# Kernel tuning notes

Measured on AMD Instinct MI355X. Metric: run time of the kernel, lower is better.

## Reference

```python
import jax, jax.numpy as jnp
import numpy as np
import math

B, N, H, OUT = 32, 2048, 256, 128
K = 6            # knn_graph k
ALPHA = 0.2      # GCN2Conv alpha (beta=1 since theta/layer are None)
NEG = 0.2        # leaky_relu negative slope in ASAP
EPS = 1e-5       # batchnorm eps
RATIOS = (0.15, 0.25, 0.5)


def _scatter_add(vals, idx, n):
    # vals [B,E] or [B,E,h], idx [B,E] -> [B,n,...]
    b, e = idx.shape
    gi = (idx + jnp.arange(b)[:, None] * n).reshape(-1)
    flat = vals.reshape((b * e,) + vals.shape[2:])
    return jax.ops.segment_sum(flat, gi, num_segments=b * n).reshape((b, n) + vals.shape[2:])


def _scatter_max(vals, idx, n):
    b, e = idx.shape
    gi = (idx + jnp.arange(b)[:, None] * n).reshape(-1)
    flat = vals.reshape((b * e,) + vals.shape[2:])
    return jax.ops.segment_max(flat, gi, num_segments=b * n).reshape((b, n) + vals.shape[2:])


def _gather(x, idx):
    # x [B,n,...] or [B,n], idx [B,E]
    if x.ndim == 3:
        return jnp.take_along_axis(x, idx[..., None], axis=1)
    return jnp.take_along_axis(x, idx, axis=1)


def _knn_undirected(pos):
    # knn_graph(pos, k=6, loop=True) then to_undirected (coalesced via `valid` mask)
    b, n, _ = pos.shape
    d2 = jnp.sum((pos[:, :, None, :] - pos[:, None, :, :]) ** 2, axis=-1)  # [B,n,n]
    _, nbr = jax.lax.top_k(-d2, K)                # self included (dist 0)
    ctr = jnp.broadcast_to(jnp.arange(n)[None, :, None], (b, n, K)).reshape(b, n * K)
    nbr = nbr.reshape(b, n * K)
    src = jnp.concatenate([nbr, ctr], axis=1)     # symmetrize
    dst = jnp.concatenate([ctr, nbr], axis=1)
    key = src * n + dst
    order = jnp.argsort(key, axis=1)
    src = jnp.take_along_axis(src, order, axis=1)
    dst = jnp.take_along_axis(dst, order, axis=1)
    key = jnp.take_along_axis(key, order, axis=1)
    valid = jnp.concatenate([jnp.ones((b, 1), bool), key[:, 1:] != key[:, :-1]], axis=1)
    return src, dst, valid


def _edge_mlp(pos, src, dst, valid, W1, b1, g, be, m, v, W2, b2):
    # relu(MLP([1,32,1])(||p_i - p_j||)); BN in eval mode; self loops replaced by 1
    d = jnp.linalg.norm(_gather(pos, src) - _gather(pos, dst), axis=-1)  # [B,E]
    t = d[..., None] @ W1 + b1                       # [B,E,32]
    t = (t - m) * jax.lax.rsqrt(v + EPS) * g + be
    t = jax.nn.relu(t)
    w = jax.nn.relu((t @ W2 + b2)[..., 0])
    w = jnp.where(src == dst, 1.0, w)                # add_remaining_self_loops fill=1
    return jnp.where(valid, w, 0.0)                  # coalesce duplicate edges


def _gcn2(x, x0, src, dst, w, Wc):
    # GCN2Conv with beta=1, shared weights: ((1-a)*A_hat x + a*x0) @ W
    n = x.shape[1]
    deg = _scatter_add(w, dst, n)
    dis = jax.lax.rsqrt(jnp.maximum(deg, 1e-12))     # deg >= 1 (self loops)
    norm = _gather(dis, src) * w * _gather(dis, dst)
    agg = _scatter_add(norm[..., None] * _gather(x, src), dst, n)
    return ((1.0 - ALPHA) * agg + ALPHA * x0) @ Wc


def _asap(x, src, dst, valid, w, kpool, Wrel, brel, Wroot, Wlin, blin, Watt, batt,
          lW1, lb1, lW2, lW3, lb3):
    n = x.shape[1]
    # gnn_intra_cluster: GraphConv (add aggregation)
    x_pool = _scatter_add(w[..., None] * _gather(x, src), dst, n) @ Wrel + brel + x @ Wroot
    mj = _gather(x_pool, src)                                    # [B,E,H]
    x_q = _scatter_max(jnp.where(valid[..., None], mj, -jnp.inf), dst, n) @ Wlin + blin
    score = (jnp.concatenate([_gather(x_q, dst), mj], axis=-1) @ Watt + batt)[..., 0]
    score = jnp.where(valid, jax.nn.leaky_relu(score, NEG), -jnp.inf)
    smax = _scatter_max(score, dst, n)
    e = jnp.where(valid, jnp.exp(score - _gather(smax, dst)), 0.0)
    att = e / _gather(_scatter_add(e, dst, n), dst)
    xn = _scatter_add(att[..., None] * _gather(x, src), dst, n)
    # LEConv fitness (no edge weights; duplicates masked)
    a = (xn @ lW1 + lb1)[..., 0]
    bb = (xn @ lW2)[..., 0]
    msg = jnp.where(valid, _gather(a, src) - _gather(bb, dst), 0.0)
    fit = jax.nn.sigmoid(_scatter_add(msg, dst, n) + (xn @ lW3 + lb3)[..., 0])
    vals, idx = jax.lax.top_k(fit, kpool)
    return _gather(xn, idx) * vals[..., None], idx


def _forward(x, pos, conv_W, eW1, eb1, ebn_g, ebn_b, ebn_m, ebn_v, eW2, eb2,
             aWrel, abrel, aWroot, aWlin, ablin, aWatt, abatt,
             leW1, leb1, leW2, leW3, leb3, gW, gb, nW, nb):
    h = None
    readouts = []
    for s in range(4):
        src, dst, valid = _knn_undirected(pos)
        w = _edge_mlp(pos, src, dst, valid, eW1[s], eb1[s], ebn_g[s], ebn_b[s],
                      ebn_m[s], ebn_v[s], eW2[s], eb2[s])
        if s in (1, 2):
            readouts.append(jnp.concatenate([jnp.mean(h, axis=1), jnp.max(h, axis=1)], axis=-1))
        hin = x if s == 0 else h
        h = jax.nn.relu(_gcn2(hin, x, src, dst, w, conv_W[s]))
        if s < 3:
            kpool = math.ceil(RATIOS[s] * h.shape[1])
            h, idx = _asap(h, src, dst, valid, w, kpool, aWrel[s], abrel[s], aWroot[s],
                           aWlin[s], ablin[s], aWatt[s], abatt[s],
                           leW1[s], leb1[s], leW2[s], leW3[s], leb3[s])
            x = _gather(x, idx)
            pos = _gather(pos, idx)
    gate = jax.nn.softmax(h @ gW + gb, axis=1)      # attentional aggregation
    gp = jnp.sum(gate * (h @ nW + nb), axis=1)      # [B,OUT]
    return jnp.concatenate([gp, readouts[1], readouts[0]], axis=-1)


def setup_inputs() -> dict:
    key = jax.random.key(0)
    ks = iter(jax.random.split(key, 40))
    def rn(shape, scale=1.0):
        return scale * jax.random.normal(next(ks), shape, dtype=jnp.float32)
    return {
        "x": rn((B, N, H)),
        "pos": rn((B, N, 3)),
        "conv_W": rn((4, H, H), H ** -0.5),
        "eW1": rn((4, 1, 32)),
        "eb1": rn((4, 32), 0.1),
        "ebn_g": 1.0 + rn((4, 32), 0.1),
        "ebn_b": rn((4, 32), 0.1),
        "ebn_m": rn((4, 32), 0.1),
        "ebn_v": jnp.ones((4, 32), jnp.float32),
        "eW2": rn((4, 32, 1), 32 ** -0.5),
        "eb2": rn((4, 1), 0.1),
        "aWrel": rn((3, H, H), H ** -0.5),
        "abrel": rn((3, H), 0.1),
        "aWroot": rn((3, H, H), H ** -0.5),
        "aWlin": rn((3, H, H), H ** -0.5),
        "ablin": rn((3, H), 0.1),
        "aWatt": rn((3, 2 * H, 1), (2 * H) ** -0.5),
        "abatt": rn((3, 1), 0.1),
        "leW1": rn((3, H, 1), H ** -0.5),
        "leb1": rn((3, 1), 0.1),
        "leW2": rn((3, H, 1), H ** -0.5),
        "leW3": rn((3, H, 1), H ** -0.5),
        "leb3": rn((3, 1), 0.1),
        "gW": rn((H, 1), H ** -0.5),
        "gb": rn((1,), 0.1),
        "nW": rn((H, OUT), H ** -0.5),
        "nb": rn((OUT,), 0.1),
    }


def reference(x, pos, conv_W, eW1, eb1, ebn_g, ebn_b, ebn_m, ebn_v, eW2, eb2,
              aWrel, abrel, aWroot, aWlin, ablin, aWatt, abatt,
              leW1, leb1, leW2, leW3, leb3, gW, gb, nW, nb):
    return _forward(x, pos, conv_W, eW1, eb1, ebn_g, ebn_b, ebn_m, ebn_v, eW2, eb2,
                    aWrel, abrel, aWroot, aWlin, ablin, aWatt, abatt,
                    leW1, leb1, leW2, leW3, leb3, gW, gb, nW, nb)
```

## Files before the change

kernel.cpp:

```cpp
#include <hip/hip_runtime.h>
#include <hip/hip_bf16.h>
#include <math.h>

#define BB 32
#define NMAX 2048
#define HD 256
#define KNN 6
#define OUTD 128
#define NCH 4

typedef __hip_bfloat16 bf16;

__global__ void k_detect(const void* __restrict__ x, int* __restrict__ flag){
  __shared__ int cnt_s;
  if (threadIdx.x==0) cnt_s=0;
  __syncthreads();
  const unsigned short* u=(const unsigned short*)x;
  int c=0;
  for (int i=threadIdx.x;i<4096;i+=256){
    int e=(u[i]>>7)&0xFF;
    if (e>=0xC0) c++;
  }
  atomicAdd(&cnt_s,c);
  __syncthreads();
  if (threadIdx.x==0) flag[0]=(cnt_s>32)?1:0;
}

__device__ __forceinline__ float loadx(const void* x, int fl, size_t idx){
  if (fl) return ((const float*)x)[idx];
  unsigned short u=((const unsigned short*)x)[idx];
  return __uint_as_float(((unsigned)u)<<16);
}

__global__ void k_cvtx(const void* __restrict__ x, const int* __restrict__ flag,
                       float* __restrict__ Hf){
  int t=blockIdx.x*256+threadIdx.x;
  Hf[t]=loadx(x,flag[0],t);
}
__global__ void k_cvtpos(const void* __restrict__ pos, const int* __restrict__ flag,
                         float* __restrict__ posF){
  int t=blockIdx.x*256+threadIdx.x;
  if (t>=BB*NMAX*3) return;
  posF[t]=loadx(pos,flag[0],t);
}
struct WTab { const void* src[25]; int cnt[25]; int dst[25]; };
__global__ void k_cvtw(WTab tab, const int* __restrict__ flag, float* __restrict__ wsW){
  int seg=blockIdx.y;
  int t=blockIdx.x*256+threadIdx.x;
  if (t>=tab.cnt[seg]) return;
  wsW[tab.dst[seg]+t]=loadx(tab.src[seg],flag[0],t);
}

__global__ void k_initcum(int* __restrict__ cum){
  int t=blockIdx.x*256+threadIdx.x;
  if (t<BB*NMAX) cum[t]=t%NMAX;
}
__global__ void k_zero2(int* __restrict__ a, int* __restrict__ b, int n){
  int t=blockIdx.x*256+threadIdx.x;
  if (t<n){ a[t]=0; b[t]=0; }
}
__global__ void k_gatherpos(const float* __restrict__ posF, const int* __restrict__ cum,
                            float* __restrict__ posf, int n){
  int t=blockIdx.x*256+threadIdx.x;
  if (t>=BB*n*3) return;
  int c=t%3, i=(t/3)%n, b=t/(3*n);
  posf[t]=posF[((size_t)b*NMAX+cum[b*NMAX+i])*3+c];
}

__global__ void k_knn_part(const float* __restrict__ posf, double* __restrict__ dcand,
                           int* __restrict__ icand, int n){
  int b=blockIdx.z, ch=blockIdx.y;
  int i=blockIdx.x*256+threadIdx.x;
  const float* pp=posf+(size_t)b*n*3;
  int cs=(n+NCH-1)/NCH;
  int jlo=ch*cs, jhi=jlo+cs; if (jhi>n) jhi=n;
  double px=0.0,py=0.0,pz=0.0;
  if (i<n){ px=(double)pp[i*3]; py=(double)pp[i*3+1]; pz=(double)pp[i*3+2]; }
  double bd0=INFINITY,bd1=INFINITY,bd2=INFINITY,bd3=INFINITY,bd4=INFINITY,bd5=INFINITY;
  int   bi0=0x7fffffff,bi1=0x7fffffff,bi2=0x7fffffff,bi3=0x7fffffff,bi4=0x7fffffff,bi5=0x7fffffff;
  __shared__ double sx[256],sy[256],sz[256];
  for (int base=jlo;base<jhi;base+=256){
    int j=base+threadIdx.x;
    if (j<jhi){ sx[threadIdx.x]=(double)pp[j*3]; sy[threadIdx.x]=(double)pp[j*3+1]; sz[threadIdx.x]=(double)pp[j*3+2]; }
    __syncthreads();
    int lim=jhi-base; if (lim>256) lim=256;
    if (i<n){
      for (int t=0;t<lim;t++){
        double dx=__dsub_rn(px,sx[t]);
        double dy=__dsub_rn(py,sy[t]);
        double dz=__dsub_rn(pz,sz[t]);
        double d2=__dadd_rn(__dadd_rn(__dmul_rn(dx,dx),__dmul_rn(dy,dy)),__dmul_rn(dz,dz));
        if (d2<bd5){
          int id=base+t;
          if (d2<bd4){ bd5=bd4; bi5=bi4;
            if (d2<bd3){ bd4=bd3; bi4=bi3;
              if (d2<bd2){ bd3=bd2; bi3=bi2;
                if (d2<bd1){ bd2=bd1; bi2=bi1;
                  if (d2<bd0){ bd1=bd0; bi1=bi0; bd0=d2; bi0=id; }
                  else { bd1=d2; bi1=id; }
                } else { bd2=d2; bi2=id; }
              } else { bd3=d2; bi3=id; }
            } else { bd4=d2; bi4=id; }
          } else { bd5=d2; bi5=id; }
        }
      }
    }
    __syncthreads();
  }
  if (i<n){
    size_t o=(((size_t)b*NCH+ch)*n+i)*KNN;
    dcand[o+0]=bd0; dcand[o+1]=bd1; dcand[o+2]=bd2; dcand[o+3]=bd3; dcand[o+4]=bd4; dcand[o+5]=bd5;
    icand[o+0]=bi0; icand[o+1]=bi1; icand[o+2]=bi2; icand[o+3]=bi3; icand[o+4]=bi4; icand[o+5]=bi5;
  }
}

__global__ void k_knn_merge(const double* __restrict__ dcand, const int* __restrict__ icand,
                            int* __restrict__ nbr, int n){
  int t=blockIdx.x*256+threadIdx.x;
  if (t>=BB*n) return;
  int b=t/n, i=t-b*n;
  double cd[NCH*KNN]; int ci[NCH*KNN];
  #pragma unroll
  for (int ch=0;ch<NCH;ch++){
    size_t o=(((size_t)b*NCH+ch)*n+i)*KNN;
    #pragma unroll
    for (int k=0;k<KNN;k++){ cd[ch*KNN+k]=dcand[o+k]; ci[ch*KNN+k]=icand[o+k]; }
  }
  int* out=nbr+(size_t)t*KNN;
  #pragma unroll
  for (int k=0;k<KNN;k++){
    int best=0;
    #pragma unroll
    for (int q=1;q<NCH*KNN;q++){
      bool lt=(cd[q]<cd[best])||(cd[q]==cd[best]&&ci[q]<ci[best]);
      if (lt) best=q;
    }
    out[k]=ci[best];
    cd[best]=INFINITY; ci[best]=0x7fffffff;
  }
}

__global__ void k_edge(const float* __restrict__ posf, const int* __restrict__ nbr,
                       float* __restrict__ w1, float* __restrict__ w2,
                       unsigned char* __restrict__ val2,
                       const float* __restrict__ W1, const float* __restrict__ b1,
                       const float* __restrict__ g,  const float* __restrict__ be,
                       const float* __restrict__ m,  const float* __restrict__ v,
                       const float* __restrict__ W2, const float* __restrict__ b2p,
                       int n){
  int t=blockIdx.x*256+threadIdx.x;
  if (t>=BB*n*KNN) return;
  int k=t%KNN; int c=(t/KNN)%n; int b=t/(KNN*n);
  const int* nb=nbr+(size_t)b*n*KNN;
  int j=nb[c*KNN+k];
  bool dup=false;
  #pragma unroll
  for (int kk=0;kk<KNN;kk++) dup=dup||(nb[j*KNN+kk]==c);
  const float* pp=posf+(size_t)b*n*3;
  double dx=__dsub_rn((double)pp[c*3+0],(double)pp[j*3+0]);
  double dy=__dsub_rn((double)pp[c*3+1],(double)pp[j*3+1]);
  double dz=__dsub_rn((double)pp[c*3+2],(double)pp[j*3+2]);
  double d2=__dadd_rn(__dadd_rn(__dmul_rn(dx,dx),__dmul_rn(dy,dy)),__dmul_rn(dz,dz));
  float dd=(float)sqrt(d2);
  float wv;
  if (j==c) wv=1.0f;
  else {
    float acc=b2p[0];
    for (int q=0;q<32;q++){
      float tt=dd*W1[q]+b1[q];
      float r=1.0f/sqrtf(v[q]+1e-5f);
      tt=(tt-m[q])*r*g[q]+be[q];
      tt=fmaxf(tt,0.f);
      acc=fmaf(tt,W2[q],acc);
    }
    wv=fmaxf(acc,0.f);
  }
  w1[t]=wv;
  w2[t]=dup?0.f:wv;
  val2[t]=dup?0:1;
}

__global__ void k_csr_count(const int* __restrict__ nbr, int* __restrict__ cnt, int n){
  int t=blockIdx.x*256+threadIdx.x;
  if (t>=BB*n*KNN) return;
  int b=t/(n*KNN);
  atomicAdd(&cnt[b*n+nbr[t]],1);
}
__global__ void k_csr_scan(const int* __restrict__ cnt, int* __restrict__ offs, int n){
  int b=blockIdx.x, t=threadIdx.x;
  int L=(n+255)/256;
  __shared__ int ssum[256];
  int lo=t*L, hi=lo+L; if (hi>n) hi=n; if (lo>n) lo=n;
  int s=0;
  for (int i=lo;i<hi;i++) s+=cnt[b*n+i];
  ssum[t]=s;
  __syncthreads();
  if (t==0){
    int run=0;
    for (int q=0;q<256;q++){ int vv=ssum[q]; ssum[q]=run; run+=vv; }
  }
  __syncthreads();
  int run=ssum[t];
  for (int i=lo;i<hi;i++){ offs[b*(n+1)+i]=run; run+=cnt[b*n+i]; }
  if (lo<n && hi==n) offs[b*(n+1)+n]=run;
}
__global__ void k_csr_fill(const int* __restrict__ nbr, const int* __restrict__ offs,
                           int* __restrict__ cur, int* __restrict__ rev, int n){
  int t=blockIdx.x*256+threadIdx.x;
  if (t>=BB*n*KNN) return;
  int b=t/(n*KNN); int rem=t-b*n*KNN;
  int d=nbr[t];
  int slot=offs[b*(n+1)+d]+atomicAdd(&cur[b*n+d],1);
  if (slot<0) slot=0;
  if (slot>=n*KNN) slot=n*KNN-1;
  rev[(size_t)b*n*KNN+slot]=rem;
}
__global__ void k_csr_sort(int* __restrict__ rev, const int* __restrict__ offs, int n){
  int t=blockIdx.x*256+threadIdx.x;
  if (t>=BB*n) return;
  int b=t/n, d=t-b*n;
  size_t base=(size_t)b*n*KNN;
  int lo=offs[b*(n+1)+d], hi=offs[b*(n+1)+d+1];
  for (int a2=lo+1;a2<hi;a2++){
    int vv=rev[base+a2]; int p=a2;
    while (p>lo && rev[base+p-1]>vv){ rev[base+p]=rev[base+p-1]; p--; }
    rev[base+p]=vv;
  }
}

__global__ void k_degdis(const float* __restrict__ w1, const float* __restrict__ w2,
                         const int* __restrict__ rev, const int* __restrict__ offs,
                         float* __restrict__ dis, int n){
  int t=blockIdx.x*256+threadIdx.x;
  if (t>=BB*n) return;
  int b=t/n, d=t-b*n;
  size_t rbase=(size_t)b*n*KNN;
  float s=0.f;
  #pragma unroll
  for (int k=0;k<KNN;k++) s+=w1[(size_t)t*KNN+k];
  int lo=offs[b*(n+1)+d], hi=offs[b*(n+1)+d+1];
  for (int sl=lo;sl<hi;sl++) s+=w2[rbase+rev[rbase+sl]];
  dis[t]=1.0f/sqrtf(fmaxf(s,1e-12f));
}

template<int MODE>
__global__ void k_nbrsum(const float* __restrict__ Hin, const float* __restrict__ w1,
                         const float* __restrict__ w2, const int* __restrict__ nbr,
                         const int* __restrict__ rev, const int* __restrict__ offs,
                         const float* __restrict__ dis, const void* __restrict__ xraw,
                         const int* __restrict__ flag,
                         const int* __restrict__ cum, float* __restrict__ outp, int n){
  int wid=blockIdx.x*4+(threadIdx.x>>6);
  int lane=threadIdx.x&63;
  if (wid>=BB*n) return;
  int b=wid/n, d=wid-b*n;
  const float* Hb=Hin+(size_t)b*n*HD;
  float a0=0,a1=0,a2=0,a3=0;
  float dd=(MODE==0)?dis[wid]:0.f;
  #pragma unroll
  for (int k=0;k<KNN;k++){
    int sN=nbr[(size_t)wid*KNN+k];
    float wv=w1[(size_t)wid*KNN+k];
    float nm=(MODE==0)?dis[b*n+sN]*wv*dd:wv;
    const float* r=Hb+(size_t)sN*HD+lane;
    a0=fmaf(nm,r[0],a0); a1=fmaf(nm,r[64],a1); a2=fmaf(nm,r[128],a2); a3=fmaf(nm,r[192],a3);
  }
  size_t rbase=(size_t)b*n*KNN;
  int lo=offs[b*(n+1)+d], hi=offs[b*(n+1)+d+1];
  for (int sl=lo;sl<hi;sl++){
    int e=rev[rbase+sl];
    int sN=e/KNN;
    float wv=w2[rbase+e];
    float nm=(MODE==0)?dis[b*n+sN]*wv*dd:wv;
    const float* r=Hb+(size_t)sN*HD+lane;
    a0=fmaf(nm,r[0],a0); a1=fmaf(nm,r[64],a1); a2=fmaf(nm,r[128],a2); a3=fmaf(nm,r[192],a3);
  }
  size_t o=(size_t)wid*HD+lane;
  if (MODE==0){
    int fl=flag[0];
    size_t xb=((size_t)b*NMAX+cum[b*NMAX+d])*HD+lane;
    a0=0.8f*a0+0.2f*loadx(xraw,fl,xb);
    a1=0.8f*a1+0.2f*loadx(xraw,fl,xb+64);
    a2=0.8f*a2+0.2f*loadx(xraw,fl,xb+128);
    a3=0.8f*a3+0.2f*loadx(xraw,fl,xb+192);
  }
  outp[o]=a0; outp[o+64]=a1; outp[o+128]=a2; outp[o+192]=a3;
}

__global__ void k_mm(const float* __restrict__ A1, const float* __restrict__ B1,
                     const float* __restrict__ A2, const float* __restrict__ B2,
                     const float* __restrict__ bias, int relu,
                     float* __restrict__ Cout, int M){
  __shared__ __align__(16) float As[16][68];
  __shared__ __align__(16) float Bs[16][260];
  int tid=threadIdx.x, bm=blockIdx.x;
  int tm=tid>>4, tn=tid&15;
  float acc[4][4][4];
  #pragma unroll
  for (int b2=0;b2<4;b2++){
    #pragma unroll
    for (int i=0;i<4;i++){
      #pragma unroll
      for (int j=0;j<4;j++) acc[b2][i][j]=0.f;
    }
  }
  int l=tid*4;
  int ar=l>>4, ak=l&15;
  int arow=bm*64+ar;
  int KT = A2 ? 512 : 256;
  for (int k0=0;k0<KT;k0+=16){
    const float* Asrc=(k0<HD)?A1:A2;
    const float* Bsrc=(k0<HD)?B1:B2;
    int kc=k0&(HD-1);
    if (arow<M){
      float4 a4=*(const float4*)(Asrc+(size_t)arow*HD+kc+ak);
      As[ak][ar]=a4.x; As[ak+1][ar]=a4.y; As[ak+2][ar]=a4.z; As[ak+3][ar]=a4.w;
    } else {
      As[ak][ar]=0.f; As[ak+1][ar]=0.f; As[ak+2][ar]=0.f; As[ak+3][ar]=0.f;
    }
    #pragma unroll
    for (int c=0;c<4;c++){
      int idx=c*256+tid;
      int rkk=idx>>6, cc=(idx&63)*4;
      *(float4*)&Bs[rkk][cc]=*(const float4*)(Bsrc+(size_t)(kc+rkk)*HD+cc);
    }
    __syncthreads();
    #pragma unroll
    for (int kk=0;kk<16;kk++){
      float4 av=*(const float4*)&As[kk][tm*4];
      #pragma unroll
      for (int b2=0;b2<4;b2++){
        float4 bv=*(const float4*)&Bs[kk][b2*64+tn*4];
        acc[b2][0][0]=fmaf(av.x,bv.x,acc[b2][0][0]); acc[b2][0][1]=fmaf(av.x,bv.y,acc[b2][0][1]);
        acc[b2][0][2]=fmaf(av.x,bv.z,acc[b2][0][2]); acc[b2][0][3]=fmaf(av.x,bv.w,acc[b2][0][3]);
        acc[b2][1][0]=fmaf(av.y,bv.x,acc[b2][1][0]); acc[b2][1][1]=fmaf(av.y,bv.y,acc[b2][1][1]);
        acc[b2][1][2]=fmaf(av.y,bv.z,acc[b2][1][2]); acc[b2][1][3]=fmaf(av.y,bv.w,acc[b2][1][3]);
        acc[b2][2][0]=fmaf(av.z,bv.x,acc[b2][2][0]); acc[b2][2][1]=fmaf(av.z,bv.y,acc[b2][2][1]);
        acc[b2][2][2]=fmaf(av.z,bv.z,acc[b2][2][2]); acc[b2][2][3]=fmaf(av.z,bv.w,acc[b2][2][3]);
        acc[b2][3][0]=fmaf(av.w,bv.x,acc[b2][3][0]); acc[b2][3][1]=fmaf(av.w,bv.y,acc[b2][3][1]);
        acc[b2][3][2]=fmaf(av.w,bv.z,acc[b2][3][2]); acc[b2][3][3]=fmaf(av.w,bv.w,acc[b2][3][3]);
      }
    }
    __syncthreads();
  }
  #pragma unroll
  for (int i=0;i<4;i++){
    int grow=bm*64+tm*4+i;
    if (grow>=M) continue;
    #pragma unroll
    for (int b2=0;b2<4;b2++){
      #pragma unroll
      for (int j=0;j<4;j++){
        int gcol=b2*64+tn*4+j;
        float v=acc[b2][i][j];
        if (bias) v+=bias[gcol];
        if (relu) v=fmaxf(v,0.f);
        Cout[(size_t)grow*HD+gcol]=v;
      }
    }
  }
}

__global__ void k_va(const float* __restrict__ Wlin, const float* __restrict__ wa,
                     const float* __restrict__ blin, float* __restrict__ va){
  int i=threadIdx.x;
  float acc=0.f;
  for (int j=0;j<HD;j++) acc=fmaf(Wlin[(size_t)i*HD+j],wa[j],acc);
  va[i]=acc;
  if (i==0){
    float c=0.f;
    for (int j=0;j<HD;j++) c=fmaf(blin[j],wa[j],c);
    va[256]=c;
  }
}

__global__ void k_qd(const float* __restrict__ T, const float* __restrict__ wb,
                     const float* __restrict__ va, const int* __restrict__ nbr,
                     const int* __restrict__ rev, const int* __restrict__ offs,
                     const unsigned char* __restrict__ val2,
                     float* __restrict__ pb, float* __restrict__ qd, int n){
  int wid=blockIdx.x*4+(threadIdx.x>>6);
  int lane=threadIdx.x&63;
  if (wid>=BB*n) return;
  int b=wid/n, d=wid-b*n;
  const float* r1=T+(size_t)wid*HD;
  float p=0.f;
  for (int h=lane;h<HD;h+=64) p=fmaf(r1[h],wb[h],p);
  const float* Tb=T+(size_t)b*n*HD;
  float m0=-INFINITY,m1=-INFINITY,m2=-INFINITY,m3=-INFINITY;
  #pragma unroll
  for (int k=0;k<KNN;k++){
    int sN=nbr[(size_t)wid*KNN+k];
    const float* r=Tb+(size_t)sN*HD+lane;
    m0=fmaxf(m0,r[0]); m1=fmaxf(m1,r[64]); m2=fmaxf(m2,r[128]); m3=fmaxf(m3,r[192]);
  }
  size_t rbase=(size_t)b*n*KNN;
  int lo=offs[b*(n+1)+d], hi=offs[b*(n+1)+d+1];
  for (int sl=lo;sl<hi;sl++){
    int e=rev[rbase+sl];
    if (!val2[rbase+e]) continue;
    int sN=e/KNN;
    const float* r=Tb+(size_t)sN*HD+lane;
    m0=fmaxf(m0,r[0]); m1=fmaxf(m1,r[64]); m2=fmaxf(m2,r[128]); m3=fmaxf(m3,r[192]);
  }
  float q=va[lane]*m0+va[lane+64]*m1+va[lane+128]*m2+va[lane+192]*m3;
  #pragma unroll
  for (int o=32;o>0;o>>=1){ p+=__shfl_xor(p,o); q+=__shfl_xor(q,o); }
  if (lane==0){ pb[wid]=p; qd[wid]=q+va[256]; }
}

__global__ void k_attxn(const float* __restrict__ Hin, const float* __restrict__ pb,
                        const float* __restrict__ qd, const int* __restrict__ nbr,
                        const int* __restrict__ rev, const int* __restrict__ offs,
                        const unsigned char* __restrict__ val2, const float* __restrict__ abatt,
                        float* __restrict__ Tout, int n){
  int wid=blockIdx.x*4+(threadIdx.x>>6);
  int lane=threadIdx.x&63;
  if (wid>=BB*n) return;
  int b=wid/n, d=wid-b*n;
  float batt=abatt[0];
  float qs=qd[wid];
  const float* Hb=Hin+(size_t)b*n*HD;
  size_t rbase=(size_t)b*n*KNN;
  int lo=offs[b*(n+1)+d], hi=offs[b*(n+1)+d+1];
  float smax=-INFINITY;
  #pragma unroll
  for (int k=0;k<KNN;k++){
    int sN=nbr[(size_t)wid*KNN+k];
    float sc=qs+pb[b*n+sN]+batt;
    sc=sc>=0.f?sc:0.2f*sc;
    smax=fmaxf(smax,sc);
  }
  for (int sl=lo;sl<hi;sl++){
    int e=rev[rbase+sl];
    if (!val2[rbase+e]) continue;
    int sN=e/KNN;
    float sc=qs+pb[b*n+sN]+batt;
    sc=sc>=0.f?sc:0.2f*sc;
    smax=fmaxf(smax,sc);
  }
  float es=0.f,a0=0,a1=0,a2=0,a3=0;
  #pragma unroll
  for (int k=0;k<KNN;k++){
    int sN=nbr[(size_t)wid*KNN+k];
    float sc=qs+pb[b*n+sN]+batt;
    sc=sc>=0.f?sc:0.2f*sc;
    float e2=expf(sc-smax);
    es+=e2;
    const float* r=Hb+(size_t)sN*HD+lane;
    a0=fmaf(e2,r[0],a0); a1=fmaf(e2,r[64],a1); a2=fmaf(e2,r[128],a2); a3=fmaf(e2,r[192],a3);
  }
  for (int sl=lo;sl<hi;sl++){
    int e=rev[rbase+sl];
    if (!val2[rbase+e]) continue;
    int sN=e/KNN;
    float sc=qs+pb[b*n+sN]+batt;
    sc=sc>=0.f?sc:0.2f*sc;
    float e2=expf(sc-smax);
    es+=e2;
    const float* r=Hb+(size_t)sN*HD+lane;
    a0=fmaf(e2,r[0],a0); a1=fmaf(e2,r[64],a1); a2=fmaf(e2,r[128],a2); a3=fmaf(e2,r[192],a3);
  }
  float inv=1.f/es;
  size_t o=(size_t)wid*HD+lane;
  Tout[o]=a0*inv; Tout[o+64]=a1*inv; Tout[o+128]=a2*inv; Tout[o+192]=a3*inv;
}

__global__ void k_ledots(const float* __restrict__ T, const float* __restrict__ lW1,
                         const float* __restrict__ lb1, const float* __restrict__ lW2,
                         const float* __restrict__ lW3, const float* __restrict__ lb3,
                         float* __restrict__ av, float* __restrict__ bbv,
                         float* __restrict__ l3v, int n){
  int wid=blockIdx.x*4+(threadIdx.x>>6);
  int lane=threadIdx.x&63;
  if (wid>=BB*n) return;
  const float* r=T+(size_t)wid*HD;
  float s1=0,s2=0,s3=0;
  for (int h=lane;h<HD;h+=64){
    float vv=r[h];
    s1=fmaf(vv,lW1[h],s1); s2=fmaf(vv,lW2[h],s2); s3=fmaf(vv,lW3[h],s3);
  }
  #pragma unroll
  for (int o=32;o>0;o>>=1){ s1+=__shfl_xor(s1,o); s2+=__shfl_xor(s2,o); s3+=__shfl_xor(s3,o); }
  if (lane==0){ av[wid]=s1+lb1[0]; bbv[wid]=s2; l3v[wid]=s3+lb3[0]; }
}

__global__ void k_fit(const float* __restrict__ av, const float* __restrict__ bbv,
                      const float* __restrict__ l3v, const int* __restrict__ nbr,
                      const int* __restrict__ rev, const int* __restrict__ offs,
                      const unsigned char* __restrict__ val2, float* __restrict__ fit, int n){
  int t=blockIdx.x*256+threadIdx.x;
  if (t>=BB*n) return;
  int b=t/n, d=t-b*n;
  size_t rbase=(size_t)b*n*KNN;
  float ms=0.f; int cv=KNN;
  #pragma unroll
  for (int k=0;k<KNN;k++) ms+=av[b*n+nbr[(size_t)t*KNN+k]];
  int lo=offs[b*(n+1)+d], hi=offs[b*(n+1)+d+1];
  for (int sl=lo;sl<hi;sl++){
    int e=rev[rbase+sl];
    if (val2[rbase+e]){ ms+=av[b*n+e/KNN]; cv++; }
  }
  float z=ms-(float)cv*bbv[t]+l3v[t];
  fit[t]=1.f/(1.f+expf(-z));
}

__global__ void k_rank(const float* __restrict__ fit, float* __restrict__ svl,
                       int* __restrict__ sid, int n, int kp){
  int t=blockIdx.x*256+threadIdx.x;
  if (t>=BB*n) return;
  int b=t/n, i=t-b*n;
  float fi=fit[t];
  const float* fb=fit+(size_t)b*n;
  int rank=0;
  for (int j=0;j<n;j++){
    float fj=fb[j];
    if (fj>fi || (fj==fi && j<i)) rank++;
  }
  if (rank<kp){ svl[b*NMAX+rank]=fi; sid[b*NMAX+rank]=i; }
}

__global__ void k_pool(const float* __restrict__ T, const float* __restrict__ svl,
                       const int* __restrict__ sid, const int* __restrict__ cumA,
                       int* __restrict__ cumB, float* __restrict__ Hout, int n, int kp){
  int wid=blockIdx.x*4+(threadIdx.x>>6);
  int lane=threadIdx.x&63;
  if (wid>=BB*kp) return;
  int b=wid/kp, j=wid-b*kp;
  int srcn=sid[b*NMAX+j];
  if (srcn<0) srcn=0;
  if (srcn>=n) srcn=n-1;
  float vv=svl[b*NMAX+j];
  const float* r=T+((size_t)b*n+srcn)*HD+lane;
  float* o=Hout+((size_t)b*kp+j)*HD+lane;
  o[0]=r[0]*vv; o[64]=r[64]*vv; o[128]=r[128]*vv; o[192]=r[192]*vv;
  if (lane==0) cumB[b*NMAX+j]=cumA[b*NMAX+srcn];
}

__global__ void k_readout(const float* __restrict__ Hb, float* __restrict__ ro, int n){
  int b=blockIdx.x, h=threadIdx.x;
  const float* p=Hb+(size_t)b*n*HD+h;
  float s=0.f, m=-INFINITY;
  for (int i=0;i<n;i++){ float v=p[(size_t)i*HD]; s+=v; m=fmaxf(m,v); }
  ro[b*512+h]=s/(float)n;
  ro[b*512+256+h]=m;
}

__global__ void k_final(const float* __restrict__ Hb, const float* __restrict__ gW,
                        const float* __restrict__ gb, const float* __restrict__ nW,
                        const float* __restrict__ nbias, const float* __restrict__ ro0,
                        const float* __restrict__ ro1, float* __restrict__ outp, int n){
  int b=blockIdx.x, tid=threadIdx.x;
  int wv=tid>>6, lane=tid&63;
  __shared__ float gate[64];
  for (int i=wv;i<n;i+=4){
    const float* r=Hb+((size_t)b*n+i)*HD;
    float p=0.f;
    for (int h=lane;h<HD;h+=64) p=fmaf(r[h],gW[h],p);
    #pragma unroll
    for (int o=32;o>0;o>>=1) p+=__shfl_xor(p,o);
    if (lane==0) gate[i]=p+gb[0];
  }
  __syncthreads();
  if (tid==0){
    float mx=-INFINITY;
    for (int i=0;i<n;i++) mx=fmaxf(mx,gate[i]);
    float sm=0.f;
    for (int i=0;i<n;i++){ gate[i]=expf(gate[i]-mx); sm+=gate[i]; }
    float inv=1.f/sm;
    for (int i=0;i<n;i++) gate[i]*=inv;
  }
  __syncthreads();
  if (tid<OUTD){
    float acc=0.f;
    for (int i=0;i<n;i++){
      const float* r=Hb+((size_t)b*n+i)*HD;
      float dot=0.f;
      for (int h=0;h<HD;h++) dot=fmaf(r[h],nW[(size_t)h*OUTD+tid],dot);
      acc=fmaf(gate[i],dot+nbias[tid],acc);
    }
    outp[(size_t)b*1152+tid]=acc;
  }
  for (int q=tid;q<512;q+=256){
    outp[(size_t)b*1152+128+q]=ro1[b*512+q];
    outp[(size_t)b*1152+640+q]=ro0[b*512+q];
  }
}

extern "C" void kernel_launch(void* const* d_in, const int* in_sizes, int n_in,
                              void* d_out, int out_size, void* d_ws, size_t ws_size,
                              hipStream_t stream){
  if (n_in<27) return;
  if (in_sizes[0]!=BB*NMAX*HD || in_sizes[1]!=BB*NMAX*3) return;
  float* outp=(float*)d_out;
  (void)out_size;

  char* p=(char*)d_ws;
  auto carve=[&](size_t bytes)->char*{ char* r=p; p+=((bytes+255)/256)*256; return r; };
  float* posF=(float*)carve((size_t)BB*NMAX*3*4);
  float* posf=(float*)carve((size_t)BB*NMAX*3*4);
  float* Hbuf=(float*)carve((size_t)BB*NMAX*HD*4);
  float* Tbuf=(float*)carve((size_t)BB*NMAX*HD*4);
  static const int wcnt[25]={262144,128,128,128,128,128,128,128,4,
                             196608,768,196608,196608,768,1536,3,
                             768,3,768,768,3,256,1,32768,128};
  int woff[25]; int wtot=0;
  for (int i=0;i<25;i++){ woff[i]=wtot; wtot+=(wcnt[i]+63)&~63; }
  float* wsW=(float*)carve((size_t)wtot*4);
  double* dcand=(double*)carve((size_t)BB*NCH*NMAX*KNN*8);
  int*    icand=(int*)  carve((size_t)BB*NCH*NMAX*KNN*4);
  int*   nbr =(int*)  carve((size_t)BB*NMAX*KNN*4);
  int*   rev =(int*)  carve((size_t)BB*NMAX*KNN*4);
  float* w1  =(float*)carve((size_t)BB*NMAX*KNN*4);
  float* w2  =(float*)carve((size_t)BB*NMAX*KNN*4);
  unsigned char* val2=(unsigned char*)carve((size_t)BB*NMAX*KNN);
  int* cnt  =(int*)carve((size_t)BB*NMAX*4);
  int* offs =(int*)carve((size_t)BB*(NMAX+1)*4);
  int* cur  =(int*)carve((size_t)BB*NMAX*4);
  float* dis=(float*)carve((size_t)BB*NMAX*4);
  float* pb =(float*)carve((size_t)BB*NMAX*4);
  float* qd =(float*)carve((size_t)BB*NMAX*4);
  float* av =(float*)carve((size_t)BB*NMAX*4);
  float* bbv=(float*)carve((size_t)BB*NMAX*4);
  float* l3v=(float*)carve((size_t)BB*NMAX*4);
  float* fit=(float*)carve((size_t)BB*NMAX*4);
  float* svl=(float*)carve((size_t)BB*NMAX*4);
  int*   sid=(int*)  carve((size_t)BB*NMAX*4);
  int* cumA =(int*)carve((size_t)BB*NMAX*4);
  int* cumB =(int*)carve((size_t)BB*NMAX*4);
  int* flag =(int*)carve(256);
  float* va =(float*)carve(272*4);
  float* ro0=(float*)carve((size_t)BB*512*4);
  float* ro1=(float*)carve((size_t)BB*512*4);
  size_t need=(size_t)(p-(char*)d_ws);
  if (ws_size<need) return;

  k_detect<<<1,256,0,stream>>>(d_in[0],flag);
  k_cvtx<<<(BB*NMAX*HD)/256,256,0,stream>>>(d_in[0],flag,Hbuf);
  k_cvtpos<<<(BB*NMAX*3+255)/256,256,0,stream>>>(d_in[1],flag,posF);
  {
    WTab tab;
    int maxc=0;
    for (int i=0;i<25;i++){ tab.src[i]=d_in[2+i]; tab.cnt[i]=wcnt[i]; tab.dst[i]=woff[i]; if (wcnt[i]>maxc) maxc=wcnt[i]; }
    k_cvtw<<<dim3((maxc+255)/256,25),256,0,stream>>>(tab,flag,wsW);
  }
  k_initcum<<<(BB*NMAX+255)/256,256,0,stream>>>(cumA);

  const int NS[4]={2048,308,77,39};
  const int KP[3]={308,77,39};

  for (int s=0;s<4;s++){
    int n=NS[s]; int M=BB*n;
    const float* wconv =wsW+woff[0]+(size_t)s*65536;
    const float* eW1p  =wsW+woff[1]+s*32;
    const float* eb1p  =wsW+woff[2]+s*32;
    const float* gp    =wsW+woff[3]+s*32;
    const float* bep   =wsW+woff[4]+s*32;
    const float* mp    =wsW+woff[5]+s*32;
    const float* vp    =wsW+woff[6]+s*32;
    const float* W2p   =wsW+woff[7]+s*32;
    const float* b2p   =wsW+woff[8]+s;
    const float* aWrelp=wsW+woff[9]+(size_t)s*65536;
    const float* abrelp=wsW+woff[10]+s*256;
    const float* aWrootp=wsW+woff[11]+(size_t)s*65536;
    const float* aWlinp=wsW+woff[12]+(size_t)s*65536;
    const float* ablinp=wsW+woff[13]+s*256;
    const float* wap   =wsW+woff[14]+s*512;
    const float* wbp   =wsW+woff[14]+s*512+256;
    const float* abattp=wsW+woff[15]+s;
    const float* leW1p =wsW+woff[16]+s*256;
    const float* leb1p =wsW+woff[17]+s;
    const float* leW2p =wsW+woff[18]+s*256;
    const float* leW3p =wsW+woff[19]+s*256;
    const float* leb3p =wsW+woff[20]+s;

    k_gatherpos<<<(BB*n*3+255)/256,256,0,stream>>>(posF,cumA,posf,n);
    k_knn_part<<<dim3((n+255)/256,NCH,BB),256,0,stream>>>(posf,dcand,icand,n);
    k_knn_merge<<<(BB*n+255)/256,256,0,stream>>>(dcand,icand,nbr,n);
    int totE=BB*n*KNN;
    k_edge<<<(totE+255)/256,256,0,stream>>>(posf,nbr,w1,w2,val2,
        eW1p,eb1p,gp,bep,mp,vp,W2p,b2p,n);
    k_zero2<<<(BB*n+255)/256,256,0,stream>>>(cnt,cur,BB*n);
    k_csr_count<<<(totE+255)/256,256,0,stream>>>(nbr,cnt,n);
    k_csr_scan<<<BB,256,0,stream>>>(cnt,offs,n);
    k_csr_fill<<<(totE+255)/256,256,0,stream>>>(nbr,offs,cur,rev,n);
    k_csr_sort<<<(BB*n+255)/256,256,0,stream>>>(rev,offs,n);
    if (s==1) k_readout<<<BB,256,0,stream>>>(Hbuf,ro0,n);
    if (s==2) k_readout<<<BB,256,0,stream>>>(Hbuf,ro1,n);
    k_degdis<<<(BB*n+255)/256,256,0,stream>>>(w1,w2,rev,offs,dis,n);
    k_nbrsum<0><<<(BB*n+3)/4,256,0,stream>>>(Hbuf,w1,w2,nbr,rev,offs,dis,d_in[0],flag,cumA,Tbuf,n);
    k_mm<<<(M+63)/64,256,0,stream>>>(Tbuf,wconv,(const float*)nullptr,(const float*)nullptr,
                                     (const float*)nullptr,1,Hbuf,M);
    if (s<3){
      int kp=KP[s];
      k_nbrsum<1><<<(BB*n+3)/4,256,0,stream>>>(Hbuf,w1,w2,nbr,rev,offs,dis,d_in[0],flag,cumA,Tbuf,n);
      k_mm<<<(M+63)/64,256,0,stream>>>(Tbuf,aWrelp,Hbuf,aWrootp,abrelp,0,Tbuf,M);
      k_va<<<1,256,0,stream>>>(aWlinp,wap,ablinp,va);
      k_qd<<<(BB*n+3)/4,256,0,stream>>>(Tbuf,wbp,va,nbr,rev,offs,val2,pb,qd,n);
      k_attxn<<<(BB*n+3)/4,256,0,stream>>>(Hbuf,pb,qd,nbr,rev,offs,val2,abattp,Tbuf,n);
      k_ledots<<<(BB*n+3)/4,256,0,stream>>>(Tbuf,leW1p,leb1p,leW2p,leW3p,leb3p,av,bbv,l3v,n);
      k_fit<<<(BB*n+255)/256,256,0,stream>>>(av,bbv,l3v,nbr,rev,offs,val2,fit,n);
      k_rank<<<(BB*n+255)/256,256,0,stream>>>(fit,svl,sid,n,kp);
      k_pool<<<(BB*kp+3)/4,256,0,stream>>>(Tbuf,svl,sid,cumA,cumB,Hbuf,n,kp);
      { int* t=cumA; cumA=cumB; cumB=t; }
    }
  }
  k_final<<<BB,256,0,stream>>>(Hbuf,wsW+woff[21],wsW+woff[22],wsW+woff[23],wsW+woff[24],
                               ro0,ro1,outp,NS[3]);
}
```

Before: 2.250 ms.

## Vectorize gathers to float4, fuse CSR count, skip x conversion, widen KNN chunks

Several changes land together. Per-row gathers in nbrsum, qd, attxn, ledots and pool now use float4 loads and stores instead of strided scalar accesses. The initial full x-to-float conversion kernel is removed, and stage 0 reads raw x directly inside nbrsum. CSR counting is folded into the edge kernel via atomics, and the KNN partition uses 8 chunks with its candidate buffers aliased into Tbuf. The risks are non-float4 bf16 loads on the raw path, a larger merge loop that is no longer unrolled, and the Tbuf aliasing.

After: 2.351 ms. +4.5%, slower.

```diff
diff --git a/kernel.cpp b/kernel.cpp
--- a/kernel.cpp
+++ b/kernel.cpp
@@ -7,7 +7,7 @@
 #define HD 256
 #define KNN 6
 #define OUTD 128
-#define NCH 4
+#define NCH 8
 
 typedef __hip_bfloat16 bf16;
 
@@ -31,12 +31,13 @@
   unsigned short u=((const unsigned short*)x)[idx];
   return __uint_as_float(((unsigned)u)<<16);
 }
-
-__global__ void k_cvtx(const void* __restrict__ x, const int* __restrict__ flag,
-                       float* __restrict__ Hf){
-  int t=blockIdx.x*256+threadIdx.x;
-  Hf[t]=loadx(x,flag[0],t);
-}
+__device__ __forceinline__ float4 loadx4(const void* x, int fl, size_t idx){
+  if (fl) return *(const float4*)((const float*)x+idx);
+  float4 r;
+  r.x=loadx(x,0,idx); r.y=loadx(x,0,idx+1); r.z=loadx(x,0,idx+2); r.w=loadx(x,0,idx+3);
+  return r;
+}
+
 __global__ void k_cvtpos(const void* __restrict__ pos, const int* __restrict__ flag,
                          float* __restrict__ posF){
   int t=blockIdx.x*256+threadIdx.x;
@@ -130,7 +131,6 @@
   #pragma unroll
   for (int k=0;k<KNN;k++){
     int best=0;
-    #pragma unroll
     for (int q=1;q<NCH*KNN;q++){
       bool lt=(cd[q]<cd[best])||(cd[q]==cd[best]&&ci[q]<ci[best]);
       if (lt) best=q;
@@ -142,7 +142,7 @@
 
 __global__ void k_edge(const float* __restrict__ posf, const int* __restrict__ nbr,
                        float* __restrict__ w1, float* __restrict__ w2,
-                       unsigned char* __restrict__ val2,
+                       unsigned char* __restrict__ val2, int* __restrict__ cnt,
                        const float* __restrict__ W1, const float* __restrict__ b1,
                        const float* __restrict__ g,  const float* __restrict__ be,
                        const float* __restrict__ m,  const float* __restrict__ v,
@@ -153,6 +153,7 @@
   int k=t%KNN; int c=(t/KNN)%n; int b=t/(KNN*n);
   const int* nb=nbr+(size_t)b*n*KNN;
   int j=nb[c*KNN+k];
+  atomicAdd(&cnt[b*n+j],1);
   bool dup=false;
   #pragma unroll
   for (int kk=0;kk<KNN;kk++) dup=dup||(nb[j*KNN+kk]==c);
@@ -180,12 +181,6 @@
   val2[t]=dup?0:1;
 }
 
-__global__ void k_csr_count(const int* __restrict__ nbr, int* __restrict__ cnt, int n){
-  int t=blockIdx.x*256+threadIdx.x;
-  if (t>=BB*n*KNN) return;
-  int b=t/(n*KNN);
-  atomicAdd(&cnt[b*n+nbr[t]],1);
-}
 __global__ void k_csr_scan(const int* __restrict__ cnt, int* __restrict__ offs, int n){
   int b=blockIdx.x, t=threadIdx.x;
   int L=(n+255)/256;
@@ -243,7 +238,7 @@
   dis[t]=1.0f/sqrtf(fmaxf(s,1e-12f));
 }
 
-template<int MODE>
+template<int MODE,int RAW>
 __global__ void k_nbrsum(const float* __restrict__ Hin, const float* __restrict__ w1,
                          const float* __restrict__ w2, const int* __restrict__ nbr,
                          const int* __restrict__ rev, const int* __restrict__ offs,
@@ -254,16 +249,19 @@
   int lane=threadIdx.x&63;
   if (wid>=BB*n) return;
   int b=wid/n, d=wid-b*n;
+  int fl=flag[0];
   const float* Hb=Hin+(size_t)b*n*HD;
-  float a0=0,a1=0,a2=0,a3=0;
+  float4 a=make_float4(0.f,0.f,0.f,0.f);
   float dd=(MODE==0)?dis[wid]:0.f;
+  int c4=lane*4;
   #pragma unroll
   for (int k=0;k<KNN;k++){
     int sN=nbr[(size_t)wid*KNN+k];
     float wv=w1[(size_t)wid*KNN+k];
     float nm=(MODE==0)?dis[b*n+sN]*wv*dd:wv;
-    const float* r=Hb+(size_t)sN*HD+lane;
-    a0=fmaf(nm,r[0],a0); a1=fmaf(nm,r[64],a1); a2=fmaf(nm,r[128],a2); a3=fmaf(nm,r[192],a3);
+    float4 r = RAW ? loadx4(xraw,fl,((size_t)b*n+sN)*HD+c4)
+                   : *(const float4*)(Hb+(size_t)sN*HD+c4);
+    a.x=fmaf(nm,r.x,a.x); a.y=fmaf(nm,r.y,a.y); a.z=fmaf(nm,r.z,a.z); a.w=fmaf(nm,r.w,a.w);
   }
   size_t rbase=(size_t)b*n*KNN;
   int lo=offs[b*(n+1)+d], hi=offs[b*(n+1)+d+1];
@@ -272,19 +270,16 @@
     int sN=e/KNN;
     float wv=w2[rbase+e];
     float nm=(MODE==0)?dis[b*n+sN]*wv*dd:wv;
-    const float* r=Hb+(size_t)sN*HD+lane;
-    a0=fmaf(nm,r[0],a0); a1=fmaf(nm,r[64],a1); a2=fmaf(nm,r[128],a2); a3=fmaf(nm,r[192],a3);
-  }
-  size_t o=(size_t)wid*HD+lane;
+    float4 r = RAW ? loadx4(xraw,fl,((size_t)b*n+sN)*HD+c4)
+                   : *(const float4*)(Hb+(size_t)sN*HD+c4);
+    a.x=fmaf(nm,r.x,a.x); a.y=fmaf(nm,r.y,a.y); a.z=fmaf(nm,r.z,a.z); a.w=fmaf(nm,r.w,a.w);
+  }
   if (MODE==0){
-    int fl=flag[0];
-    size_t xb=((size_t)b*NMAX+cum[b*NMAX+d])*HD+lane;
-    a0=0.8f*a0+0.2f*loadx(xraw,fl,xb);
-    a1=0.8f*a1+0.2f*loadx(xraw,fl,xb+64);
-    a2=0.8f*a2+0.2f*loadx(xraw,fl,xb+128);
-    a3=0.8f*a3+0.2f*loadx(xraw,fl,xb+192);
-  }
-  outp[o]=a0; outp[o+64]=a1; outp[o+128]=a2; outp[o+192]=a3;
+    float4 xr=loadx4(xraw,fl,((size_t)b*NMAX+cum[b*NMAX+d])*HD+c4);
+    a.x=0.8f*a.x+0.2f*xr.x; a.y=0.8f*a.y+0.2f*xr.y;
+    a.z=0.8f*a.z+0.2f*xr.z; a.w=0.8f*a.w+0.2f*xr.w;
+  }
+  *(float4*)(outp+(size_t)wid*HD+c4)=a;
 }
 
 __global__ void k_mm(const float* __restrict__ A1, const float* __restrict__ B1,
@@ -383,16 +378,17 @@
   int lane=threadIdx.x&63;
   if (wid>=BB*n) return;
   int b=wid/n, d=wid-b*n;
-  const float* r1=T+(size_t)wid*HD;
-  float p=0.f;
-  for (int h=lane;h<HD;h+=64) p=fmaf(r1[h],wb[h],p);
+  int c4=lane*4;
+  float4 r1=*(const float4*)(T+(size_t)wid*HD+c4);
+  float4 wb4=*(const float4*)(wb+c4);
+  float p=r1.x*wb4.x+r1.y*wb4.y+r1.z*wb4.z+r1.w*wb4.w;
   const float* Tb=T+(size_t)b*n*HD;
-  float m0=-INFINITY,m1=-INFINITY,m2=-INFINITY,m3=-INFINITY;
+  float4 m4=make_float4(-INFINITY,-INFINITY,-INFINITY,-INFINITY);
   #pragma unroll
   for (int k=0;k<KNN;k++){
     int sN=nbr[(size_t)wid*KNN+k];
-    const float* r=Tb+(size_t)sN*HD+lane;
-    m0=fmaxf(m0,r[0]); m1=fmaxf(m1,r[64]); m2=fmaxf(m2,r[128]); m3=fmaxf(m3,r[192]);
+    float4 r=*(const float4*)(Tb+(size_t)sN*HD+c4);
+    m4.x=fmaxf(m4.x,r.x); m4.y=fmaxf(m4.y,r.y); m4.z=fmaxf(m4.z,r.z); m4.w=fmaxf(m4.w,r.w);
   }
   size_t rbase=(size_t)b*n*KNN;
   int lo=offs[b*(n+1)+d], hi=offs[b*(n+1)+d+1];
@@ -400,10 +396,11 @@
     int e=rev[rbase+sl];
     if (!val2[rbase+e]) continue;
     int sN=e/KNN;
-    const float* r=Tb+(size_t)sN*HD+lane;
-    m0=fmaxf(m0,r[0]); m1=fmaxf(m1,r[64]); m2=fmaxf(m2,r[128]); m3=fmaxf(m3,r[192]);
-  }
-  float q=va[lane]*m0+va[lane+64]*m1+va[lane+128]*m2+va[lane+192]*m3;
+    float4 r=*(const float4*)(Tb+(size_t)sN*HD+c4);
+    m4.x=fmaxf(m4.x,r.x); m4.y=fmaxf(m4.y,r.y); m4.z=fmaxf(m4.z,r.z); m4.w=fmaxf(m4.w,r.w);
+  }
+  float4 va4=*(const float4*)(va+c4);
+  float q=va4.x*m4.x+va4.y*m4.y+va4.z*m4.z+va4.w*m4.w;
   #pragma unroll
   for (int o=32;o>0;o>>=1){ p+=__shfl_xor(p,o); q+=__shfl_xor(q,o); }
   if (lane==0){ pb[wid]=p; qd[wid]=q+va[256]; }
@@ -421,6 +418,7 @@
   float batt=abatt[0];
   float qs=qd[wid];
   const float* Hb=Hin+(size_t)b*n*HD;
+  int c4=lane*4;
   size_t rbase=(size_t)b*n*KNN;
   int lo=offs[b*(n+1)+d], hi=offs[b*(n+1)+d+1];
   float smax=-INFINITY;
@@ -439,7 +437,8 @@
     sc=sc>=0.f?sc:0.2f*sc;
     smax=fmaxf(smax,sc);
   }
-  float es=0.f,a0=0,a1=0,a2=0,a3=0;
+  float es=0.f;
+  float4 a=make_float4(0.f,0.f,0.f,0.f);
   #pragma unroll
   for (int k=0;k<KNN;k++){
     int sN=nbr[(size_t)wid*KNN+k];
@@ -447,8 +446,8 @@
     sc=sc>=0.f?sc:0.2f*sc;
     float e2=expf(sc-smax);
     es+=e2;
-    const float* r=Hb+(size_t)sN*HD+lane;
-    a0=fmaf(e2,r[0],a0); a1=fmaf(e2,r[64],a1); a2=fmaf(e2,r[128],a2); a3=fmaf(e2,r[192],a3);
+    float4 r=*(const float4*)(Hb+(size_t)sN*HD+c4);
+    a.x=fmaf(e2,r.x,a.x); a.y=fmaf(e2,r.y,a.y); a.z=fmaf(e2,r.z,a.z); a.w=fmaf(e2,r.w,a.w);
   }
   for (int sl=lo;sl<hi;sl++){
     int e=rev[rbase+sl];
@@ -458,12 +457,12 @@
     sc=sc>=0.f?sc:0.2f*sc;
     float e2=expf(sc-smax);
     es+=e2;
-    const float* r=Hb+(size_t)sN*HD+lane;
-    a0=fmaf(e2,r[0],a0); a1=fmaf(e2,r[64],a1); a2=fmaf(e2,r[128],a2); a3=fmaf(e2,r[192],a3);
+    float4 r=*(const float4*)(Hb+(size_t)sN*HD+c4);
+    a.x=fmaf(e2,r.x,a.x); a.y=fmaf(e2,r.y,a.y); a.z=fmaf(e2,r.z,a.z); a.w=fmaf(e2,r.w,a.w);
   }
   float inv=1.f/es;
-  size_t o=(size_t)wid*HD+lane;
-  Tout[o]=a0*inv; Tout[o+64]=a1*inv; Tout[o+128]=a2*inv; Tout[o+192]=a3*inv;
+  a.x*=inv; a.y*=inv; a.z*=inv; a.w*=inv;
+  *(float4*)(Tout+(size_t)wid*HD+c4)=a;
 }
 
 __global__ void k_ledots(const float* __restrict__ T, const float* __restrict__ lW1,
@@ -474,12 +473,14 @@
   int wid=blockIdx.x*4+(threadIdx.x>>6);
   int lane=threadIdx.x&63;
   if (wid>=BB*n) return;
-  const float* r=T+(size_t)wid*HD;
-  float s1=0,s2=0,s3=0;
-  for (int h=lane;h<HD;h+=64){
-    float vv=r[h];
-    s1=fmaf(vv,lW1[h],s1); s2=fmaf(vv,lW2[h],s2); s3=fmaf(vv,lW3[h],s3);
-  }
+  int c4=lane*4;
+  float4 r=*(const float4*)(T+(size_t)wid*HD+c4);
+  float4 w1v=*(const float4*)(lW1+c4);
+  float4 w2v=*(const float4*)(lW2+c4);
+  float4 w3v=*(const float4*)(lW3+c4);
+  float s1=r.x*w1v.x+r.y*w1v.y+r.z*w1v.z+r.w*w1v.w;
+  float s2=r.x*w2v.x+r.y*w2v.y+r.z*w2v.z+r.w*w2v.w;
+  float s3=r.x*w3v.x+r.y*w3v.y+r.z*w3v.z+r.w*w3v.w;
   #pragma unroll
   for (int o=32;o>0;o>>=1){ s1+=__shfl_xor(s1,o); s2+=__shfl_xor(s2,o); s3+=__shfl_xor(s3,o); }
   if (lane==0){ av[wid]=s1+lb1[0]; bbv[wid]=s2; l3v[wid]=s3+lb3[0]; }
@@ -531,9 +532,10 @@
   if (srcn<0) srcn=0;
   if (srcn>=n) srcn=n-1;
   float vv=svl[b*NMAX+j];
-  const float* r=T+((size_t)b*n+srcn)*HD+lane;
-  float* o=Hout+((size_t)b*kp+j)*HD+lane;
-  o[0]=r[0]*vv; o[64]=r[64]*vv; o[128]=r[128]*vv; o[192]=r[192]*vv;
+  int c4=lane*4;
+  float4 r=*(const float4*)(T+((size_t)b*n+srcn)*HD+c4);
+  r.x*=vv; r.y*=vv; r.z*=vv; r.w*=vv;
+  *(float4*)(Hout+((size_t)b*kp+j)*HD+c4)=r;
   if (lane==0) cumB[b*NMAX+j]=cumA[b*NMAX+srcn];
 }
 
@@ -607,8 +609,6 @@
   int woff[25]; int wtot=0;
   for (int i=0;i<25;i++){ woff[i]=wtot; wtot+=(wcnt[i]+63)&~63; }
   float* wsW=(float*)carve((size_t)wtot*4);
-  double* dcand=(double*)carve((size_t)BB*NCH*NMAX*KNN*8);
-  int*    icand=(int*)  carve((size_t)BB*NCH*NMAX*KNN*4);
   int*   nbr =(int*)  carve((size_t)BB*NMAX*KNN*4);
   int*   rev =(int*)  carve((size_t)BB*NMAX*KNN*4);
   float* w1  =(float*)carve((size_t)BB*NMAX*KNN*4);
@@ -635,8 +635,10 @@
   size_t need=(size_t)(p-(char*)d_ws);
   if (ws_size<need) return;
 
+  double* dcand=(double*)Tbuf;
+  int*    icand=(int*)((char*)Tbuf + (size_t)BB*NCH*NMAX*KNN*8);
+
   k_detect<<<1,256,0,stream>>>(d_in[0],flag);
-  k_cvtx<<<(BB*NMAX*HD)/256,256,0,stream>>>(d_in[0],flag,Hbuf);
   k_cvtpos<<<(BB*NMAX*3+255)/256,256,0,stream>>>(d_in[1],flag,posF);
   {
     WTab tab;
@@ -678,22 +680,24 @@
     k_knn_part<<<dim3((n+255)/256,NCH,BB),256,0,stream>>>(posf,dcand,icand,n);
     k_knn_merge<<<(BB*n+255)/256,256,0,stream>>>(dcand,icand,nbr,n);
     int totE=BB*n*KNN;
-    k_edge<<<(totE+255)/256,256,0,stream>>>(posf,nbr,w1,w2,val2,
+    k_zero2<<<(BB*n+255)/256,256,0,stream>>>(cnt,cur,BB*n);
+    k_edge<<<(totE+255)/256,256,0,stream>>>(posf,nbr,w1,w2,val2,cnt,
         eW1p,eb1p,gp,bep,mp,vp,W2p,b2p,n);
-    k_zero2<<<(BB*n+255)/256,256,0,stream>>>(cnt,cur,BB*n);
-    k_csr_count<<<(totE+255)/256,256,0,stream>>>(nbr,cnt,n);
     k_csr_scan<<<BB,256,0,stream>>>(cnt,offs,n);
     k_csr_fill<<<(totE+255)/256,256,0,stream>>>(nbr,offs,cur,rev,n);
     k_csr_sort<<<(BB*n+255)/256,256,0,stream>>>(rev,offs,n);
     if (s==1) k_readout<<<BB,256,0,stream>>>(Hbuf,ro0,n);
     if (s==2) k_readout<<<BB,256,0,stream>>>(Hbuf,ro1,n);
     k_degdis<<<(BB*n+255)/256,256,0,stream>>>(w1,w2,rev,offs,dis,n);
-    k_nbrsum<0><<<(BB*n+3)/4,256,0,stream>>>(Hbuf,w1,w2,nbr,rev,offs,dis,d_in[0],flag,cumA,Tbuf,n);
+    if (s==0)
+      k_nbrsum<0,1><<<(BB*n+3)/4,256,0,stream>>>(nullptr,w1,w2,nbr,rev,offs,dis,d_in[0],flag,cumA,Tbuf,n);
+    else
+      k_nbrsum<0,0><<<(BB*n+3)/4,256,0,stream>>>(Hbuf,w1,w2,nbr,rev,offs,dis,d_in[0],flag,cumA,Tbuf,n);
     k_mm<<<(M+63)/64,256,0,stream>>>(Tbuf,wconv,(const float*)nullptr,(const float*)nullptr,
                                      (const float*)nullptr,1,Hbuf,M);
     if (s<3){
       int kp=KP[s];
-      k_nbrsum<1><<<(BB*n+3)/4,256,0,stream>>>(Hbuf,w1,w2,nbr,rev,offs,dis,d_in[0],flag,cumA,Tbuf,n);
+      k_nbrsum<1,0><<<(BB*n+3)/4,256,0,stream>>>(Hbuf,w1,w2,nbr,rev,offs,dis,d_in[0],flag,cumA,Tbuf,n);
       k_mm<<<(M+63)/64,256,0,stream>>>(Tbuf,aWrelp,Hbuf,aWrootp,abrelp,0,Tbuf,M);
       k_va<<<1,256,0,stream>>>(aWlinp,wap,ablinp,va);
       k_qd<<<(BB*n+3)/4,256,0,stream>>>(Tbuf,wbp,va,nbr,rev,offs,val2,pb,qd,n);
```
